# Kernel optimization log

Hardware: AMD Instinct MI355X
Metric: run time of the kernel (lower is better)

Reference implementation:

```python
import jax, jax.numpy as jnp
import numpy as np
from jax.ops import segment_sum, segment_max

B = 512          # parcels (batch of graphs)
P = 200          # poi nodes per parcel
N = B * P        # total poi nodes
E_POI = N * 16   # intra-parcel poi graph edges
HID = 256
IN_CH = 64
HEADS = 3
OUT = 12
T0 = 0.9
SLOPE = 0.2      # GATConv leaky_relu negative slope
NODE_GRAPH = jnp.arange(N, dtype=jnp.int32) // P  # poi node -> parcel id
ARANGE_N = jnp.arange(N, dtype=jnp.int32)


def setup_inputs() -> dict:
    key = jax.random.key(0)
    ks = jax.random.split(key, 24)
    g = lambda i, shape: jax.random.normal(ks[i], shape, jnp.float32) * 0.05
    # poi graph edges constrained within each parcel block
    src0 = jax.random.randint(ks[0], (E_POI,), 0, N, dtype=jnp.int32)
    off = jax.random.randint(ks[1], (E_POI,), 0, P, dtype=jnp.int32)
    return dict(
        g_poi_features=jax.random.normal(ks[2], (N, IN_CH), jnp.float32),
        img_feat=jax.random.normal(ks[3], (B, 2048), jnp.float32),
        edge_src=src0,
        edge_dst=(src0 // P) * P + off,
        W_gcn1=g(4, (IN_CH, HID)), b_gcn1=jnp.zeros((HID,), jnp.float32),
        W_gcn2=g(5, (HID, HID)), b_gcn2=jnp.zeros((HID,), jnp.float32),
        W_hrs=g(6, (2048, HID)), b_hrs=jnp.zeros((HID,), jnp.float32),
        W_proj_hrs=g(7, (HID, HID)), b_proj_hrs=jnp.zeros((HID,), jnp.float32),
        W_proj_poi=g(8, (HID, HID)), b_proj_poi=jnp.zeros((HID,), jnp.float32),
        W_gat_in=g(9, (HID, HEADS * HID)), al_in=g(10, (HEADS, HID)), ar_in=g(11, (HEADS, HID)),
        W_gat_with=g(12, (HID, HEADS * HID)), al_with=g(13, (HEADS, HID)), ar_with=g(14, (HEADS, HID)),
        W_hrsgnn=g(15, (HID, HID)),
        W_poignn=g(16, (HID, HID)),
        W_fc=g(17, (4 * HID, OUT)), b_fc=jnp.zeros((OUT,), jnp.float32),
    )


def _gcn(x, src, dst, W, b):
    # DGL GraphConv, norm='both', self-loops added
    s = jnp.concatenate([src, ARANGE_N])
    d = jnp.concatenate([dst, ARANGE_N])
    deg = segment_sum(jnp.ones_like(s, jnp.float32), d, num_segments=N)
    norm = jax.lax.rsqrt(jnp.maximum(deg, 1.0))
    h = (x @ W) * norm[:, None]
    m = segment_sum(h[s], d, num_segments=N)
    return m * norm[:, None] + b


def _gat(h_src, h_dst, src, dst, n_dst, W, al, ar):
    # DGL GATConv math: shared fc, additive attention, edge-softmax over dst
    fs = (h_src @ W).reshape(-1, HEADS, HID)
    fd = (h_dst @ W).reshape(-1, HEADS, HID)
    el = (fs * al).sum(-1)   # [n_src, H]
    er = (fd * ar).sum(-1)   # [n_dst, H]
    e = el[src] + er[dst]
    e = jnp.where(e > 0, e, SLOPE * e)
    m = segment_max(e, dst, num_segments=n_dst)
    w = jnp.exp(e - m[dst])
    z = segment_sum(w, dst, num_segments=n_dst)
    alpha = w / (z[dst] + 1e-9)
    out = segment_sum(fs[src] * alpha[:, :, None], dst, num_segments=n_dst)
    return out.mean(1)  # mean over heads (parcel_output.mean(1) in source)


def _mean_nodes(x):
    # dgl.mean_nodes over uniform-size batched graphs
    return segment_sum(x, NODE_GRAPH, num_segments=B) / P


def reference(g_poi_features, img_feat, edge_src, edge_dst,
              W_gcn1, b_gcn1, W_gcn2, b_gcn2, W_hrs, b_hrs,
              W_proj_hrs, b_proj_hrs, W_proj_poi, b_proj_poi,
              W_gat_in, al_in, ar_in, W_gat_with, al_with, ar_with,
              W_hrsgnn, W_poignn, W_fc, b_fc):
    # hrs_encoder: ResNet50 backbone modeled as precomputed 2048-d feats + replaced fc
    hrs = img_feat @ W_hrs + b_hrs                                  # [B, HID]
    # poi_encoder: 2-layer GCN over batched poi graph
    x = jax.nn.relu(_gcn(g_poi_features, edge_src, edge_dst, W_gcn1, b_gcn1))
    poi_nodes = _gcn(x, edge_src, edge_dst, W_gcn2, b_gcn2)         # [N, HID]
    poi_pooled = _mean_nodes(poi_nodes)                             # [B, HID]
    # mid-level fused similarity
    med = jnp.concatenate([hrs, poi_pooled], axis=1)
    med = med / jnp.linalg.norm(med, axis=1, keepdims=True)
    med_output = (med @ med.T + 1.0) / 2.0                          # [B, B]
    # UniSimGraph: GCN on thresholded parcel-similarity graph
    adj = jnp.where(med_output >= T0, 1.0, 0.0)
    adj = jnp.maximum(adj, jnp.eye(B, dtype=jnp.float32))
    dinv = jax.lax.rsqrt(adj.sum(1))
    nadj = adj * dinv[:, None] * dinv[None, :]
    hrs_agg = jax.nn.relu(nadj @ (hrs @ W_hrsgnn))                  # [B, HID]
    poi_agg = jax.nn.relu(nadj @ (poi_pooled @ W_poignn))           # [B, HID]
    # getHetGraph: bipartite poi<->parcel GAT, 3 heads, sum-aggregate, head-mean
    ph = hrs @ W_proj_hrs + b_proj_hrs                              # parcel feats
    pp = poi_nodes @ W_proj_poi + b_proj_poi                        # poi feats
    poi2img = _gat(pp, ph, ARANGE_N, NODE_GRAPH, B, W_gat_in, al_in, ar_in)      # [B, HID]
    img2poi = _gat(ph, pp, NODE_GRAPH, ARANGE_N, N, W_gat_with, al_with, ar_with)  # [N, HID]
    img2poi_pooled = _mean_nodes(img2poi)                           # [B, HID]
    # MutualAgg concat order: [img2poi, poi2poi(=poi_agg), poi2img, img2img(=hrs_agg)]
    agg = jnp.concatenate([img2poi_pooled, poi_agg, poi2img, hrs_agg], axis=1)
    output = agg @ W_fc + b_fc                                      # [B, OUT]
    return (output, med_output)
```

## Files before the change

### kernel.cpp

```cpp
#include <hip/hip_runtime.h>
#include <hip/hip_bf16.h>
#include <math.h>


#define N_NODES 102400
#define B_PAR   512
#define P_NODES 200
#define E_EDGES 1638400
#define HIDF    256

typedef __attribute__((ext_vector_type(8))) short bf16x8;
typedef __attribute__((ext_vector_type(4))) float f32x4;

__device__ __forceinline__ unsigned short f2bf(float x) {
    unsigned u = __builtin_bit_cast(unsigned, x);
    u += 0x7fffu + ((u >> 16) & 1u);
    return (unsigned short)(u >> 16);
}
__device__ __forceinline__ float bf2f(unsigned short h) {
    return __builtin_bit_cast(float, (unsigned)h << 16);
}
__device__ __forceinline__ int lds_off(int row, int kbyte) {
    return row * 128 + ((((kbyte >> 4) ^ (row & 7)) << 4) | (kbyte & 15));
}
template<bool BF16SRC>
__device__ __forceinline__ bf16x8 load_row8(const void* p, size_t elemoff) {
    if constexpr (BF16SRC) {
        return *(const bf16x8*)((const unsigned short*)p + elemoff);
    } else {
        const float* ap = (const float*)p + elemoff;
        float4 lo = *(const float4*)ap;
        float4 hi = *(const float4*)(ap + 4);
        union { bf16x8 v; unsigned short u[8]; } pk;
        pk.u[0] = f2bf(lo.x); pk.u[1] = f2bf(lo.y);
        pk.u[2] = f2bf(lo.z); pk.u[3] = f2bf(lo.w);
        pk.u[4] = f2bf(hi.x); pk.u[5] = f2bf(hi.y);
        pk.u[6] = f2bf(hi.z); pk.u[7] = f2bf(hi.w);
        return pk.v;
    }
}
__device__ __forceinline__ bf16x8 u8x8_to_bf16(uint2 w) {
    union { bf16x8 v; unsigned short u[8]; } r;
#pragma unroll
    for (int b = 0; b < 4; ++b) {
        r.u[b]     = (unsigned short)(__builtin_bit_cast(unsigned,
                        (float)((w.x >> (8 * b)) & 255u)) >> 16);
        r.u[4 + b] = (unsigned short)(__builtin_bit_cast(unsigned,
                        (float)((w.y >> (8 * b)) & 255u)) >> 16);
    }
    return r.v;
}

__global__ __launch_bounds__(512, 2) void gcnA_k(
    const unsigned char* __restrict__ Adj, const float* __restrict__ gp,
    const float* __restrict__ nrm, const unsigned short* __restrict__ W1t,
    const float* __restrict__ b1, unsigned short* __restrict__ X1nT)
{
    __shared__ unsigned short lds[256 * 72];
    unsigned short* XnT = lds;
    unsigned short* AX1 = lds;

    const int tid  = threadIdx.x;
    const int p    = blockIdx.x;
    const int lane = tid & 63;
    const int wave = tid >> 6;
    const int frow = lane & 15;
    const int fq   = lane >> 4;
    const int r4   = fq << 2;
    const f32x4 fz = {0.f, 0.f, 0.f, 0.f};

    uint2 adjr[2][7];
#pragma unroll
    for (int mi = 0; mi < 2; ++mi) {
        const unsigned char* ar = Adj + ((size_t)p << 16)
            + (size_t)(wave * 32 + mi * 16 + frow) * 256 + fq * 8;
#pragma unroll
        for (int ks = 0; ks < 7; ++ks)
            adjr[mi][ks] = *(const uint2*)(ar + ks * 32);
    }
    bf16x8 w1f[2][2];
#pragma unroll
    for (int mi = 0; mi < 2; ++mi)
#pragma unroll
        for (int ks = 0; ks < 2; ++ks)
            w1f[mi][ks] = *(const bf16x8*)(W1t
                + (size_t)(wave * 32 + mi * 16 + frow) * 64 + ks * 32 + fq * 8);

    for (int idx = tid; idx < 224 * 16; idx += 512) {
        int s = idx >> 4, kc = idx & 15;
        float4 v = {0.f, 0.f, 0.f, 0.f};
        float nr = 0.f;
        if (s < 200) {
            v = *(const float4*)(gp + ((size_t)(p * 200 + s)) * 64 + kc * 4);
            nr = nrm[p * 200 + s];
        }
        XnT[(kc * 4 + 0) * 232 + s] = f2bf(v.x * nr);
        XnT[(kc * 4 + 1) * 232 + s] = f2bf(v.y * nr);
        XnT[(kc * 4 + 2) * 232 + s] = f2bf(v.z * nr);
        XnT[(kc * 4 + 3) * 232 + s] = f2bf(v.w * nr);
    }
    __syncthreads();

    f32x4 acc2[2][4];
#pragma unroll
    for (int i = 0; i < 2; ++i)
#pragma unroll
        for (int j = 0; j < 4; ++j) acc2[i][j] = fz;
#pragma unroll
    for (int ks = 0; ks < 7; ++ks) {
        bf16x8 a0 = u8x8_to_bf16(adjr[0][ks]);
        bf16x8 a1 = u8x8_to_bf16(adjr[1][ks]);
#pragma unroll
        for (int ni = 0; ni < 4; ++ni) {
            bf16x8 bfr = *(const bf16x8*)(XnT
                + (size_t)(ni * 16 + frow) * 232 + ks * 32 + fq * 8);
            acc2[0][ni] = __builtin_amdgcn_mfma_f32_16x16x32_bf16(a0, bfr, acc2[0][ni], 0, 0, 0);
            acc2[1][ni] = __builtin_amdgcn_mfma_f32_16x16x32_bf16(a1, bfr, acc2[1][ni], 0, 0, 0);
        }
    }
    __syncthreads();
#pragma unroll
    for (int mi = 0; mi < 2; ++mi)
#pragma unroll
        for (int ni = 0; ni < 4; ++ni)
#pragma unroll
            for (int j = 0; j < 4; ++j)
                AX1[(size_t)(wave * 32 + mi * 16 + r4 + j) * 72 + ni * 16 + frow]
                    = f2bf(acc2[mi][ni][j]);
    __syncthreads();

    f32x4 acc3[2][16];
#pragma unroll
    for (int i = 0; i < 2; ++i)
#pragma unroll
        for (int j = 0; j < 16; ++j) acc3[i][j] = fz;
#pragma unroll
    for (int ks = 0; ks < 2; ++ks)
#pragma unroll
        for (int ni = 0; ni < 16; ++ni) {
            bf16x8 bfr = *(const bf16x8*)(AX1
                + (size_t)(ni * 16 + frow) * 72 + ks * 32 + fq * 8);
            acc3[0][ni] = __builtin_amdgcn_mfma_f32_16x16x32_bf16(w1f[0][ks], bfr, acc3[0][ni], 0, 0, 0);
            acc3[1][ni] = __builtin_amdgcn_mfma_f32_16x16x32_bf16(w1f[1][ks], bfr, acc3[1][ni], 0, 0, 0);
        }

    float nrd[16];
#pragma unroll
    for (int ni = 0; ni < 16; ++ni) {
        int d = ni * 16 + frow;
        nrd[ni] = (d < 200) ? nrm[p * 200 + d] : 0.f;
    }
#pragma unroll
    for (int mi = 0; mi < 2; ++mi)
#pragma unroll
        for (int j = 0; j < 4; ++j) {
            int f = wave * 32 + mi * 16 + r4 + j;
            float bv = b1[f];
#pragma unroll
            for (int ni = 0; ni < 16; ++ni) {
                int d = ni * 16 + frow;
                if (d < 224) {
                    float v = fmaxf(acc3[mi][ni][j] * nrd[ni] + bv, 0.f) * nrd[ni];
                    X1nT[((size_t)p * 256 + f) * 224 + d] = f2bf(v);
                }
            }
        }
}

__global__ __launch_bounds__(512, 2) void gcnB_k(
    const unsigned char* __restrict__ Adj, const unsigned short* __restrict__ X1nT,
    const unsigned short* __restrict__ W2t, const float* __restrict__ nrm,
    const float* __restrict__ b2, unsigned short* __restrict__ PN,
    float* __restrict__ pool, unsigned short* __restrict__ poolb)
{
    __shared__ unsigned short Bb[32 * 232];
    __shared__ unsigned short AXb[256 * 40];
    __shared__ unsigned short W2b[256 * 40];
    __shared__ float poolsh[256];

    const int tid  = threadIdx.x;
    const int p    = blockIdx.x;
    const int lane = tid & 63;
    const int wave = tid >> 6;
    const int frow = lane & 15;
    const int fq   = lane >> 4;
    const int r4   = fq << 2;
    const f32x4 fz = {0.f, 0.f, 0.f, 0.f};

    if (tid < 256) poolsh[tid] = 0.f;

    bf16x8 adjb[2][7];
#pragma unroll
    for (int mi = 0; mi < 2; ++mi) {
        const unsigned char* ar = Adj + ((size_t)p << 16)
            + (size_t)(wave * 32 + mi * 16 + frow) * 256 + fq * 8;
#pragma unroll
        for (int ks = 0; ks < 7; ++ks)
            adjb[mi][ks] = u8x8_to_bf16(*(const uint2*)(ar + ks * 32));
    }

    f32x4 acc5[2][16];
#pragma unroll
    for (int i = 0; i < 2; ++i)
#pragma unroll
        for (int j = 0; j < 16; ++j) acc5[i][j] = fz;

#pragma unroll
    for (int i = 0; i < 2; ++i) {
        int idx = tid + i * 512;
        if (idx < 896) {
            int r = idx / 28, ch = idx - r * 28;
            *(uint4*)(Bb + r * 232 + ch * 8) =
                *(const uint4*)(X1nT + ((size_t)p * 256 + r) * 224 + ch * 8);
        }
        int r2 = idx >> 2, ch2 = idx & 3;
        *(uint4*)(W2b + r2 * 40 + ch2 * 8) =
            *(const uint4*)(W2t + (size_t)r2 * 256 + ch2 * 8);
    }
    __syncthreads();

    for (int c = 0; c < 8; ++c) {
        uint4 stb[2];
#pragma unroll
        for (int i = 0; i < 2; ++i) {
            int idx = tid + i * 512;
            if (c < 7 && idx < 896) {
                int r = idx / 28, ch = idx - r * 28;
                stb[i] = *(const uint4*)(X1nT
                    + ((size_t)p * 256 + (c + 1) * 32 + r) * 224 + ch * 8);
            }
        }
        f32x4 acc4[2][2];
#pragma unroll
        for (int i = 0; i < 2; ++i)
#pragma unroll
            for (int j = 0; j < 2; ++j) acc4[i][j] = fz;
#pragma unroll
        for (int ks = 0; ks < 7; ++ks)
#pragma unroll
            for (int ni = 0; ni < 2; ++ni) {
                bf16x8 bfr = *(const bf16x8*)(Bb
                    + (size_t)(ni * 16 + frow) * 232 + ks * 32 + fq * 8);
                acc4[0][ni] = __builtin_amdgcn_mfma_f32_16x16x32_bf16(adjb[0][ks], bfr, acc4[0][ni], 0, 0, 0);
                acc4[1][ni] = __builtin_amdgcn_mfma_f32_16x16x32_bf16(adjb[1][ks], bfr, acc4[1][ni], 0, 0, 0);
            }
        __syncthreads();
#pragma unroll
        for (int mi = 0; mi < 2; ++mi)
#pragma unroll
            for (int ni = 0; ni < 2; ++ni)
#pragma unroll
                for (int j = 0; j < 4; ++j)
                    AXb[(size_t)(wave * 32 + mi * 16 + r4 + j) * 40 + ni * 16 + frow]
                        = f2bf(acc4[mi][ni][j]);
#pragma unroll
        for (int i = 0; i < 2; ++i) {
            int idx = tid + i * 512;
            if (c < 7 && idx < 896) {
                int r = idx / 28, ch = idx - r * 28;
                *(uint4*)(Bb + r * 232 + ch * 8) = stb[i];
            }
        }
        __syncthreads();
        uint4 stw[2];
#pragma unroll
        for (int i = 0; i < 2; ++i) {
            int idx = tid + i * 512;
            int r = idx >> 2, ch = idx & 3;
            if (c < 7)
                stw[i] = *(const uint4*)(W2t
                    + (size_t)r * 256 + (c + 1) * 32 + ch * 8);
        }
        bf16x8 af[2];
        af[0] = *(const bf16x8*)(AXb + (size_t)(wave * 32 + frow) * 40 + fq * 8);
        af[1] = *(const bf16x8*)(AXb + (size_t)(wave * 32 + 16 + frow) * 40 + fq * 8);
#pragma unroll
        for (int ni = 0; ni < 16; ++ni) {
            bf16x8 bfr = *(const bf16x8*)(W2b + (size_t)(ni * 16 + frow) * 40 + fq * 8);
            acc5[0][ni] = __builtin_amdgcn_mfma_f32_16x16x32_bf16(af[0], bfr, acc5[0][ni], 0, 0, 0);
            acc5[1][ni] = __builtin_amdgcn_mfma_f32_16x16x32_bf16(af[1], bfr, acc5[1][ni], 0, 0, 0);
        }
        __syncthreads();
#pragma unroll
        for (int i = 0; i < 2; ++i) {
            int idx = tid + i * 512;
            int r = idx >> 2, ch = idx & 3;
            if (c < 7) *(uint4*)(W2b + r * 40 + ch * 8) = stw[i];
        }
    }

    float b2v[16], psum[16];
#pragma unroll
    for (int ni = 0; ni < 16; ++ni) {
        b2v[ni] = b2[ni * 16 + frow];
        psum[ni] = 0.f;
    }
#pragma unroll
    for (int mi = 0; mi < 2; ++mi)
#pragma unroll
        for (int j = 0; j < 4; ++j) {
            int d = wave * 32 + mi * 16 + r4 + j;
            if (d < 200) {
                int g = p * 200 + d;
                float nr = nrm[g];
#pragma unroll
                for (int ni = 0; ni < 16; ++ni) {
                    float v = acc5[mi][ni][j] * nr + b2v[ni];
                    PN[(size_t)g * 256 + ni * 16 + frow] = f2bf(v);
                    psum[ni] += v;
                }
            }
        }
#pragma unroll
    for (int ni = 0; ni < 16; ++ni) {
        float s = psum[ni];
        s += __shfl_xor(s, 16);
        s += __shfl_xor(s, 32);
        if (fq == 0) atomicAdd(&poolsh[ni * 16 + frow], s);
    }
    __syncthreads();
    if (tid < 256) {
        float pv = poolsh[tid] * (1.f / 200.f);
        pool[(size_t)p * 256 + tid] = pv;
        poolb[(size_t)p * 256 + tid] = f2bf(pv);
    }
}

template<bool ABF16, bool BBF16, int OMODE, bool BIASF, bool RELUF,
         bool MEDOUT, int KCHUNK>
__global__ __launch_bounds__(256) void mm64_k(
    const void* __restrict__ Ain, const void* __restrict__ Bin,
    void* __restrict__ Cout, int M, int Nc, int K,
    const float* __restrict__ bias, float alpha)
{
    __shared__ bf16x8 smem_v[1024];
    unsigned char* Asm = (unsigned char*)smem_v;
    unsigned char* Bsm = Asm + 8192;

    const int tid  = threadIdx.x;
    const int m0   = blockIdx.y * 64;
    const int n0   = blockIdx.x * 64;
    const int sr   = tid >> 3, sc = tid & 7;
    const int lane = tid & 63;
    const int wm   = (tid >> 7) & 1, wn = (tid >> 6) & 1;
    const int frow = lane & 15;
    const int fko  = (lane >> 4) << 4;

    int kbeg = 0, kend = K;
    float* Cf = (float*)Cout;
    if (KCHUNK > 0) {
        kbeg = blockIdx.z * KCHUNK; kend = kbeg + KCHUNK;
        Cf += (size_t)blockIdx.z * M * Nc;
    }

    f32x4 acc[2][2];
    const f32x4 fz = {0.f, 0.f, 0.f, 0.f};
#pragma unroll
    for (int i = 0; i < 2; ++i)
#pragma unroll
        for (int j = 0; j < 2; ++j) acc[i][j] = fz;

    bf16x8 areg[2], breg[2];
    auto load_tiles = [&](int k0) {
#pragma unroll
        for (int i = 0; i < 2; ++i) {
            int row = sr + 32 * i;
            areg[i] = load_row8<ABF16>(Ain, (size_t)(m0 + row) * K + k0 + sc * 8);
            breg[i] = load_row8<BBF16>(Bin, (size_t)(n0 + row) * K + k0 + sc * 8);
        }
    };

    load_tiles(kbeg);
    for (int k0 = kbeg; k0 < kend; k0 += 64) {
        __syncthreads();
#pragma unroll
        for (int i = 0; i < 2; ++i) {
            *(bf16x8*)(Asm + lds_off(sr + 32 * i, sc * 16)) = areg[i];
            *(bf16x8*)(Bsm + lds_off(sr + 32 * i, sc * 16)) = breg[i];
        }
        __syncthreads();
        if (k0 + 64 < kend) load_tiles(k0 + 64);
#pragma unroll
        for (int ks = 0; ks < 2; ++ks) {
            const int kb = ks * 64 + fko;
            bf16x8 af[2], bfr[2];
#pragma unroll
            for (int t = 0; t < 2; ++t)
                af[t] = *(const bf16x8*)(Asm + lds_off(wm * 32 + t * 16 + frow, kb));
#pragma unroll
            for (int t = 0; t < 2; ++t)
                bfr[t] = *(const bf16x8*)(Bsm + lds_off(wn * 32 + t * 16 + frow, kb));
#pragma unroll
            for (int mi = 0; mi < 2; ++mi)
#pragma unroll
                for (int ni = 0; ni < 2; ++ni)
                    acc[mi][ni] = __builtin_amdgcn_mfma_f32_16x16x32_bf16(
                        af[mi], bfr[ni], acc[mi][ni], 0, 0, 0);
        }
    }

    const int r4 = (lane >> 4) << 2;
#pragma unroll
    for (int mi = 0; mi < 2; ++mi) {
#pragma unroll
        for (int ni = 0; ni < 2; ++ni) {
            int col = n0 + wn * 32 + ni * 16 + frow;
#pragma unroll
            for (int j = 0; j < 4; ++j) {
                int row = m0 + wm * 32 + mi * 16 + r4 + j;
                float v = acc[mi][ni][j] * alpha;
                if (BIASF)  v += bias[col];
                if (RELUF)  v = fmaxf(v, 0.f);
                if (MEDOUT) v += 0.5f;
                if (OMODE == 0) {
                    Cf[(size_t)row * Nc + col] = v;
                } else {
                    ((unsigned short*)Cout)[(size_t)row * Nc + col] = f2bf(v);
                }
            }
        }
    }
}

__global__ __launch_bounds__(256) void edge_diag_k(
    const int* __restrict__ esrc, const int* __restrict__ edst,
    unsigned char* __restrict__ A)
{
    int id = blockIdx.x * 256 + threadIdx.x;
    size_t bo;
    if (id < E_EDGES) {
        int s = esrc[id], d = edst[id];
        int p = d / 200;
        int dl = d - p * 200, sl = s - p * 200;
        bo = (((size_t)(p * 256 + dl)) << 8) + (unsigned)sl;
    } else {
        int i2 = id - E_EDGES;
        int p = i2 / 200, d = i2 - p * 200;
        bo = (((size_t)(p * 256 + d)) << 8) + (unsigned)d;
    }
    atomicAdd((unsigned int*)(A + (bo & ~(size_t)3)), 1u << ((bo & 3) * 8));
}

__global__ __launch_bounds__(256) void norm2_k(const unsigned char* __restrict__ A,
                                               float* __restrict__ nrm)
{
    int g = blockIdx.x * 256 + threadIdx.x;
    int p = g / 200, d = g - p * 200;
    const uint4* row = (const uint4*)(A + (((size_t)(p * 256 + d)) << 8));
    unsigned s = 0;
#pragma unroll
    for (int i = 0; i < 16; ++i) {
        uint4 w = row[i];
        unsigned a = w.x, b = w.y, c = w.z, e = w.w;
        s += (a & 255) + ((a >> 8) & 255) + ((a >> 16) & 255) + (a >> 24);
        s += (b & 255) + ((b >> 8) & 255) + ((b >> 16) & 255) + (b >> 24);
        s += (c & 255) + ((c >> 8) & 255) + ((c >> 16) & 255) + (c >> 24);
        s += (e & 255) + ((e >> 8) & 255) + ((e >> 16) & 255) + (e >> 24);
    }
    nrm[g] = rsqrtf((float)s);
}

__global__ __launch_bounds__(256) void prep_k(
    const float* __restrict__ W1, const float* __restrict__ W2,
    const float* __restrict__ Whg,
    const float* __restrict__ Wpg, const float* __restrict__ Whrs,
    const float* __restrict__ Wgin, const float* __restrict__ Wgw,
    const float* __restrict__ Wph, const float* __restrict__ img,
    unsigned short* __restrict__ W1t, unsigned short* __restrict__ W2t,
    unsigned short* __restrict__ Whgt,
    unsigned short* __restrict__ Wpgt, unsigned short* __restrict__ Whrst,
    unsigned short* __restrict__ Wgint, unsigned short* __restrict__ Wmt,
    unsigned short* __restrict__ Wphb, unsigned short* __restrict__ imgb)
{
    int b = blockIdx.x, tid = threadIdx.x;
    if (b < 64) {
        int id = b * 256 + tid; int n = id >> 6, k = id & 63;
        W1t[id] = f2bf(W1[(size_t)k * 256 + n]);
// ... 51 lines not shown
        bgg[j] = s * (1.f / 3.f);
    }
}

__global__ __launch_bounds__(256) void hrs_reduce_k(
    const float* __restrict__ part, const float* __restrict__ bhrs,
    float* __restrict__ hrs, unsigned short* __restrict__ hrsb)
{
    int id = blockIdx.x * 256 + threadIdx.x;
    float s = bhrs[id & 255];
#pragma unroll
    for (int z = 0; z < 8; ++z) s += part[(size_t)z * 131072 + id];
    hrs[id] = s;
    hrsb[id] = f2bf(s);
}

__global__ __launch_bounds__(256) void med_build_k(
    const float* __restrict__ hrs, const float* __restrict__ pool,
    unsigned short* __restrict__ medb)
{
    __shared__ float red[256];
    int b = blockIdx.x, f = threadIdx.x;
    float v0 = hrs[(size_t)b * 256 + f];
    float v1 = pool[(size_t)b * 256 + f];
    red[f] = v0 * v0 + v1 * v1;
    __syncthreads();
    for (int s = 128; s > 0; s >>= 1) {
        if (f < s) red[f] += red[f + s];
        __syncthreads();
    }
    float inv = rsqrtf(red[0]);
    medb[(size_t)b * 512 + f]       = f2bf(v0 * inv);
    medb[(size_t)b * 512 + 256 + f] = f2bf(v1 * inv);
}

__global__ __launch_bounds__(256) void dinv_k(const float* __restrict__ mo,
                                              float* __restrict__ dinv)
{
    __shared__ int red[256];
    int i = blockIdx.x, t = threadIdx.x;
    int c = 0;
    for (int j = t; j < 512; j += 256) c += (mo[(size_t)i * 512 + j] >= 0.9f) ? 1 : 0;
    red[t] = c; __syncthreads();
    for (int s = 128; s > 0; s >>= 1) {
        if (t < s) red[t] += red[t + s];
        __syncthreads();
    }
    if (t == 0) dinv[i] = rsqrtf((float)red[0]);
}

__global__ __launch_bounds__(256) void nadj_k(const float* __restrict__ mo,
                                              const float* __restrict__ dinv,
                                              unsigned short* __restrict__ nadjb)
{
    int i = blockIdx.x, t = threadIdx.x;
    float di = dinv[i];
    for (int j = t; j < 512; j += 256) {
        float a = (mo[(size_t)i * 512 + j] >= 0.9f || j == i) ? 1.f : 0.f;
        nadjb[(size_t)i * 512 + j] = f2bf(a * di * dinv[j]);
    }
}

__global__ __launch_bounds__(256) void uv1_k(
    const float* __restrict__ Wgin, const float* __restrict__ al,
    const float* __restrict__ ar,
    float* __restrict__ u2, float* __restrict__ v2)
{
    const int wave = threadIdx.x >> 6, lane = threadIdx.x & 63;
    const int task = blockIdx.x * 4 + wave;
    const int k = task / 3, h = task - k * 3;
    float4 w = *(const float4*)(Wgin + (size_t)k * 768 + h * 256 + lane * 4);
    float4 a = *(const float4*)(al + h * 256 + lane * 4);
    float4 r = *(const float4*)(ar + h * 256 + lane * 4);
    float su = w.x * a.x + w.y * a.y + w.z * a.z + w.w * a.w;
    float sv = w.x * r.x + w.y * r.y + w.z * r.z + w.w * r.w;
#pragma unroll
    for (int o = 32; o > 0; o >>= 1) {
        su += __shfl_xor(su, o);
        sv += __shfl_xor(sv, o);
    }
    if (lane == 0) { u2[task] = su; v2[task] = sv; }
}

__global__ __launch_bounds__(256) void uv2_k(
    const float* __restrict__ Wph, const float* __restrict__ Wpp,
    const float* __restrict__ bph, const float* __restrict__ bpp,
    const unsigned short* __restrict__ Wmt,
    const float* __restrict__ u2, const float* __restrict__ v2,
    float* __restrict__ vv2, float* __restrict__ wu,
    float* __restrict__ bc, float* __restrict__ erb, float* __restrict__ eb0)
{
    __shared__ float ush[768], vsh[768];
    const int tid = threadIdx.x;
    for (int i = tid; i < 768; i += 256) { ush[i] = u2[i]; vsh[i] = v2[i]; }
    __syncthreads();
    const int wave = tid >> 6, lane = tid & 63;
    const int task = blockIdx.x * 4 + wave;
    float s = 0.f;
    if (task < 1536) {
        int t2 = task < 768 ? task : task - 768;
        int k = t2 / 3, h = t2 - k * 3;
        const float* W = task < 768 ? Wph : Wpp;
        const float* vec = task < 768 ? vsh : ush;
        float4 w = *(const float4*)(W + (size_t)k * 256 + lane * 4);
        s = w.x * vec[(lane * 4 + 0) * 3 + h] + w.y * vec[(lane * 4 + 1) * 3 + h]
          + w.z * vec[(lane * 4 + 2) * 3 + h] + w.w * vec[(lane * 4 + 3) * 3 + h];
#pragma unroll
        for (int o = 32; o > 0; o >>= 1) s += __shfl_xor(s, o);
        if (lane == 0) { if (task < 768) vv2[t2] = s; else wu[t2] = s; }
    } else if (task < 1792) {
        int k = task - 1536;
        float4 b4 = *(const float4*)(bph + lane * 4);
        const unsigned short* wm = Wmt + (size_t)k * 256 + lane * 4;
        s = b4.x * bf2f(wm[0]) + b4.y * bf2f(wm[1])
          + b4.z * bf2f(wm[2]) + b4.w * bf2f(wm[3]);
#pragma unroll
        for (int o = 32; o > 0; o >>= 1) s += __shfl_xor(s, o);
        if (lane == 0) bc[k] = s;
    } else if (task < 1798) {
        int t2 = task - 1792;
        int h = t2 % 3;
        bool second = t2 >= 3;
        const float* bias = second ? bpp : bph;
        const float* vec  = second ? ush : vsh;
        float4 b4 = *(const float4*)(bias + lane * 4);
        s = b4.x * vec[(lane * 4 + 0) * 3 + h] + b4.y * vec[(lane * 4 + 1) * 3 + h]
          + b4.z * vec[(lane * 4 + 2) * 3 + h] + b4.w * vec[(lane * 4 + 3) * 3 + h];
#pragma unroll
        for (int o = 32; o > 0; o >>= 1) s += __shfl_xor(s, o);
        if (lane == 0) { if (second) eb0[h] = s; else erb[h] = s; }
    }
}

__global__ __launch_bounds__(256) void er2_k(
    const float* __restrict__ hrs, const float* __restrict__ vv2,
    const float* __restrict__ erb, const float* __restrict__ eb0,
    float* __restrict__ er)
{
    __shared__ float vsh[768];
    const int tid = threadIdx.x;
    for (int i = tid; i < 768; i += 256) vsh[i] = vv2[i];
    __syncthreads();
    const int wave = tid >> 6, lane = tid & 63;
    const int task = blockIdx.x * 4 + wave;
    const int b = task / 3, h = task - b * 3;
    float4 hv = *(const float4*)(hrs + (size_t)b * 256 + lane * 4);
    float s = hv.x * vsh[(lane * 4 + 0) * 3 + h] + hv.y * vsh[(lane * 4 + 1) * 3 + h]
            + hv.z * vsh[(lane * 4 + 2) * 3 + h] + hv.w * vsh[(lane * 4 + 3) * 3 + h];
#pragma unroll
    for (int o = 32; o > 0; o >>= 1) s += __shfl_xor(s, o);
    if (lane == 0) er[task] = erb[h] + eb0[h] + s;
}

__global__ __launch_bounds__(256) void gat_poi2img_k(
    const unsigned short* __restrict__ PN, const float* __restrict__ wu,
    const float* __restrict__ er, float* __restrict__ q)
{
    __shared__ float esh[600];
    __shared__ float ash[600];
    __shared__ float ush[768];
    __shared__ float mz[8];
    const int p = blockIdx.x, tid = threadIdx.x;
    const size_t base = (size_t)p * P_NODES;

    for (int i = tid; i < 768; i += 256) ush[i] = wu[i];
    __syncthreads();

    for (int it = tid; it < 600; it += 256) {
        int n = it / 3, h = it % 3;
        const unsigned short* row = PN + (base + n) * HIDF;
        float s = 0.f;
        for (int k = 0; k < 256; k += 8) {
            union { uint4 qv; unsigned short us[8]; } w;
            w.qv = *(const uint4*)(row + k);
#pragma unroll
            for (int j = 0; j < 8; ++j) s += bf2f(w.us[j]) * ush[(k + j) * 3 + h];
        }
        s += er[p * 3 + h];
        esh[it] = s > 0.f ? s : 0.2f * s;
    }
    __syncthreads();

    int wave = tid >> 6, lane = tid & 63;
    if (wave < 3) {
        float mx = -1e30f;
        for (int n = lane; n < P_NODES; n += 64) mx = fmaxf(mx, esh[n * 3 + wave]);
        for (int o = 32; o > 0; o >>= 1) mx = fmaxf(mx, __shfl_xor(mx, o));
        float sm = 0.f;
        for (int n = lane; n < P_NODES; n += 64) sm += expf(esh[n * 3 + wave] - mx);
        for (int o = 32; o > 0; o >>= 1) sm += __shfl_xor(sm, o);
        if (lane == 0) { mz[wave] = mx; mz[4 + wave] = sm; }
    }
    __syncthreads();

    for (int it = tid; it < 600; it += 256) {
        int h = it % 3;
        ash[it] = expf(esh[it] - mz[h]) / (mz[4 + h] + 1e-9f);
    }
    __syncthreads();

    float a0 = 0.f, a1 = 0.f, a2 = 0.f;
    for (int n = 0; n < P_NODES; ++n) {
        float vv = bf2f(PN[(base + n) * HIDF + tid]);
        a0 += ash[n * 3 + 0] * vv;
        a1 += ash[n * 3 + 1] * vv;
        a2 += ash[n * 3 + 2] * vv;
    }
    q[((size_t)p * 3 + 0) * 256 + tid] = a0;
    q[((size_t)p * 3 + 1) * 256 + tid] = a1;
    q[((size_t)p * 3 + 2) * 256 + tid] = a2;
}

__global__ __launch_bounds__(256) void final_k(
    const float* __restrict__ i2p, const float* __restrict__ hpagg,
    const float* __restrict__ p2i,
    const float* __restrict__ Wfc, const float* __restrict__ bfc,
    float* __restrict__ out)
{
    int id = blockIdx.x * 256 + threadIdx.x;
    if (id >= B_PAR * 12) return;
    int b = id / 12, o = id % 12;
    float acc = bfc[o];
    const float* s0 = i2p + (size_t)b * 256;
    const float* s1 = hpagg + (size_t)b * 512 + 256;
    const float* s2 = p2i + (size_t)b * 256;
    const float* s3 = hpagg + (size_t)b * 512;
    for (int k = 0; k < 256; ++k) {
        acc += s0[k] * Wfc[(size_t)(0 * 256 + k) * 12 + o];
        acc += s1[k] * Wfc[(size_t)(1 * 256 + k) * 12 + o];
        acc += s2[k] * Wfc[(size_t)(2 * 256 + k) * 12 + o];
        acc += s3[k] * Wfc[(size_t)(3 * 256 + k) * 12 + o];
    }
    out[id] = acc;
}

extern "C" void kernel_launch(void* const* d_in, const int* in_sizes, int n_in,
                              void* d_out, int out_size, void* d_ws, size_t ws_size,
                              hipStream_t stream)
{
    const float* g_poi = (const float*)d_in[0];
    const float* img   = (const float*)d_in[1];
    const int*   esrc  = (const int*)d_in[2];
    const int*   edst  = (const int*)d_in[3];
    const float* W1    = (const float*)d_in[4];
    const float* b1    = (const float*)d_in[5];
    const float* W2    = (const float*)d_in[6];
    const float* b2    = (const float*)d_in[7];
    const float* Whrs  = (const float*)d_in[8];
    const float* bhrs  = (const float*)d_in[9];
    const float* Wph   = (const float*)d_in[10];
    const float* bph   = (const float*)d_in[11];
    const float* Wpp   = (const float*)d_in[12];
    const float* bpp   = (const float*)d_in[13];
    const float* Wgin  = (const float*)d_in[14];
    const float* alin  = (const float*)d_in[15];
    const float* arin  = (const float*)d_in[16];
    const float* Wgw   = (const float*)d_in[17];
    const float* Whg   = (const float*)d_in[20];
    const float* Wpg   = (const float*)d_in[21];
    const float* Wfc   = (const float*)d_in[22];
    const float* bfc   = (const float*)d_in[23];

    float* out     = (float*)d_out;
    float* med_out = out + B_PAR * 12;

    char* ws = (char*)d_ws;
    size_t off = 0;
    auto take = [&](size_t bytes) { void* pv = ws + off; off += (bytes + 255) & ~(size_t)255; return pv; };

    unsigned char*  adj8 = (unsigned char*)take((size_t)B_PAR * 256 * 256);
    unsigned short* X1nT = (unsigned short*)take((size_t)B_PAR * 256 * 224 * 2);
    unsigned short* XPN  = (unsigned short*)take((size_t)N_NODES * 256 * 2);
    float*          part = (float*)take((size_t)8 * 512 * 256 * 4);

    unsigned short* W1t   = (unsigned short*)take(256 * 64 * 2);
    unsigned short* W2t   = (unsigned short*)take(256 * 256 * 2);
    unsigned short* Whgt  = (unsigned short*)take(256 * 256 * 2);
    unsigned short* Wpgt  = (unsigned short*)take(256 * 256 * 2);
    unsigned short* Whrst = (unsigned short*)take((size_t)256 * 2048 * 2);
    unsigned short* Wgint = (unsigned short*)take((size_t)256 * 768 * 2);
    unsigned short* Wmt   = (unsigned short*)take(256 * 256 * 2);
    unsigned short* Wphb  = (unsigned short*)take(256 * 256 * 2);
    unsigned short* WcT   = (unsigned short*)take(256 * 256 * 2);
    unsigned short* WpG   = (unsigned short*)take((size_t)256 * 768 * 2);
    unsigned short* imgb  = (unsigned short*)take((size_t)512 * 2048 * 2);
    unsigned short* hrsb  = (unsigned short*)take((size_t)B_PAR * 256 * 2);
    unsigned short* poolb = (unsigned short*)take((size_t)B_PAR * 256 * 2);
    unsigned short* medb  = (unsigned short*)take((size_t)B_PAR * 512 * 2);
    unsigned short* nadjb = (unsigned short*)take((size_t)B_PAR * 512 * 2);
    unsigned short* Tcatt = (unsigned short*)take((size_t)512 * 512 * 2);
    float* nrm   = (float*)take((size_t)N_NODES * 4);
    float* hrs   = (float*)take((size_t)B_PAR * 256 * 4);
    float* pool  = (float*)take((size_t)B_PAR * 256 * 4);
    float* dinv  = (float*)take((size_t)B_PAR * 4);
    float* hpagg = (float*)take((size_t)B_PAR * 512 * 4);
    float* u2    = (float*)take(768 * 4);
    float* v2    = (float*)take(768 * 4);
    float* wu    = (float*)take(768 * 4);
    float* vv2   = (float*)take(768 * 4);
    float* erb   = (float*)take(16);
    float* eb0   = (float*)take(16);
    float* bc    = (float*)take(256 * 4);
    float* bgg   = (float*)take(256 * 4);
    float* er    = (float*)take((size_t)B_PAR * 3 * 4);
    float* q     = (float*)take((size_t)B_PAR * 768 * 4);
    float* p2i   = (float*)take((size_t)B_PAR * 256 * 4);
    float* i2p   = (float*)take((size_t)B_PAR * 256 * 4);
    (void)ws_size; (void)in_sizes; (void)n_in; (void)out_size;

    hipMemsetAsync(adj8, 0, (size_t)B_PAR * 256 * 256, stream);
    prep_k<<<8256, 256, 0, stream>>>(W1, W2, Whg, Wpg, Whrs, Wgin, Wgw,
        Wph, img, W1t, W2t, Whgt, Wpgt, Whrst, Wgint, Wmt, Wphb, imgb);
    edge_diag_k<<<(E_EDGES + N_NODES) / 256, 256, 0, stream>>>(esrc, edst, adj8);
    norm2_k<<<N_NODES / 256, 256, 0, stream>>>(adj8, nrm);
    wpg_k<<<769, 256, 0, stream>>>(Wpp, Wgin, bpp, WpG, bgg);

    mm64_k<true, true, 0, false, false, false, 256>
        <<<dim3(4, 8, 8), 256, 0, stream>>>(imgb, Whrst, part, 512, 256, 2048,
            nullptr, 1.f);
    hrs_reduce_k<<<512, 256, 0, stream>>>(part, bhrs, hrs, hrsb);

    uv1_k<<<192, 256, 0, stream>>>(Wgin, alin, arin, u2, v2);
    uv2_k<<<450, 256, 0, stream>>>(Wph, Wpp, bph, bpp, Wmt, u2, v2,
                                   vv2, wu, bc, erb, eb0);
    er2_k<<<384, 256, 0, stream>>>(hrs, vv2, erb, eb0, er);
    mm64_k<true, true, 1, false, false, false, 0>
        <<<dim3(4, 4), 256, 0, stream>>>(Wmt, Wphb, WcT, 256, 256, 256,
            nullptr, 1.f);

    gcnA_k<<<B_PAR, 512, 0, stream>>>(adj8, g_poi, nrm, W1t, b1, X1nT);
    gcnB_k<<<B_PAR, 512, 0, stream>>>(adj8, X1nT, W2t, nrm, b2, XPN,
                                      pool, poolb);

    med_build_k<<<B_PAR, 256, 0, stream>>>(hrs, pool, medb);
    mm64_k<true, true, 0, false, false, true, 0>
        <<<dim3(8, 8), 256, 0, stream>>>(medb, medb, med_out, 512, 512, 512,
            nullptr, 0.5f);

    dinv_k<<<B_PAR, 256, 0, stream>>>(med_out, dinv);
    nadj_k<<<B_PAR, 256, 0, stream>>>(med_out, dinv, nadjb);
    mm64_k<true, true, 1, false, false, false, 0>
        <<<dim3(8, 4), 256, 0, stream>>>(Whgt, hrsb, Tcatt, 256, 512, 256,
            nullptr, 1.f);
    mm64_k<true, true, 1, false, false, false, 0>
        <<<dim3(8, 4), 256, 0, stream>>>(Wpgt, poolb, Tcatt + (size_t)256 * 512,
            256, 512, 256, nullptr, 1.f);
    mm64_k<true, true, 0, false, true, false, 0>
        <<<dim3(8, 8), 256, 0, stream>>>(nadjb, Tcatt, hpagg, 512, 512, 512,
            nullptr, 1.f);

    gat_poi2img_k<<<B_PAR, 256, 0, stream>>>(XPN, wu, er, q);
    mm64_k<false, true, 0, true, false, false, 0>
        <<<dim3(4, 8), 256, 0, stream>>>(q, WpG, p2i, 512, 256, 768,
            bgg, 1.f / 3.f);

    mm64_k<true, true, 0, true, false, false, 0>
        <<<dim3(4, 8), 256, 0, stream>>>(hrsb, WcT, i2p, 512, 256, 256,
            bc, 1.f);

    final_k<<<24, 256, 0, stream>>>(i2p, hpagg, p2i, Wfc, bfc, out);
}
```

Before: 391.6 us.

## Fuse GAT poi-to-parcel attention into second GCN kernel and swizzle LDS layouts

```diff
diff --git a/kernel.cpp b/kernel.cpp
--- a/kernel.cpp
+++ b/kernel.cpp
@@ -22,6 +22,9 @@
 }
 __device__ __forceinline__ int lds_off(int row, int kbyte) {
     return row * 128 + ((((kbyte >> 4) ^ (row & 7)) << 4) | (kbyte & 15));
+}
+__device__ __forceinline__ int w2off(int row, int kbyte) {
+    return row * 64 + (((((kbyte >> 4) & 3) ^ (row & 3)) << 4) | (kbyte & 15));
 }
 template<bool BF16SRC>
 __device__ __forceinline__ bf16x8 load_row8(const void* p, size_t elemoff) {
@@ -50,15 +53,20 @@
     }
     return r.v;
 }
+__device__ __forceinline__ unsigned long long pack4bf(f32x4 v) {
+    union { unsigned long long u; unsigned short h[4]; } pk;
+    pk.h[0] = f2bf(v[0]); pk.h[1] = f2bf(v[1]);
+    pk.h[2] = f2bf(v[2]); pk.h[3] = f2bf(v[3]);
+    return pk.u;
+}
 
 __global__ __launch_bounds__(512, 2) void gcnA_k(
     const unsigned char* __restrict__ Adj, const float* __restrict__ gp,
     const float* __restrict__ nrm, const unsigned short* __restrict__ W1t,
     const float* __restrict__ b1, unsigned short* __restrict__ X1nT)
 {
-    __shared__ unsigned short lds[256 * 72];
-    unsigned short* XnT = lds;
-    unsigned short* AX1 = lds;
+    __shared__ unsigned char XnU[32768];
+    __shared__ unsigned char AXU[32768];
 
     const int tid  = threadIdx.x;
     const int p    = blockIdx.x;
@@ -86,60 +94,52 @@
             w1f[mi][ks] = *(const bf16x8*)(W1t
                 + (size_t)(wave * 32 + mi * 16 + frow) * 64 + ks * 32 + fq * 8);
 
-    for (int idx = tid; idx < 224 * 16; idx += 512) {
-        int s = idx >> 4, kc = idx & 15;
-        float4 v = {0.f, 0.f, 0.f, 0.f};
-        float nr = 0.f;
-        if (s < 200) {
-            v = *(const float4*)(gp + ((size_t)(p * 200 + s)) * 64 + kc * 4);
-            nr = nrm[p * 200 + s];
-        }
-        XnT[(kc * 4 + 0) * 232 + s] = f2bf(v.x * nr);
-        XnT[(kc * 4 + 1) * 232 + s] = f2bf(v.y * nr);
-        XnT[(kc * 4 + 2) * 232 + s] = f2bf(v.z * nr);
-        XnT[(kc * 4 + 3) * 232 + s] = f2bf(v.w * nr);
+    for (int gi = wave; gi < 28; gi += 8) {
+        int s0 = gi * 8;
+        union { bf16x8 v; unsigned short h[8]; } pk;
+#pragma unroll
+        for (int t = 0; t < 8; ++t) {
+            int s = s0 + t;
+            float val = 0.f;
+            if (s < 200)
+                val = gp[((size_t)(p * 200 + s)) * 64 + lane] * nrm[p * 200 + s];
+            pk.h[t] = f2bf(val);
+        }
+        *(bf16x8*)(XnU + lds_off((s0 >> 6) * 64 + lane, (s0 & 63) * 2)) = pk.v;
     }
     __syncthreads();
 
-    f32x4 acc2[2][4];
+#pragma unroll
+    for (int mi_d = 0; mi_d < 2; ++mi_d) {
+        bf16x8 adjf[7];
+#pragma unroll
+        for (int ks = 0; ks < 7; ++ks) adjf[ks] = u8x8_to_bf16(adjr[mi_d][ks]);
+#pragma unroll
+        for (int kt = 0; kt < 4; ++kt) {
+            f32x4 a2 = fz;
+#pragma unroll
+            for (int ks = 0; ks < 7; ++ks) {
+                bf16x8 af = *(const bf16x8*)(XnU + lds_off(
+                    (ks >> 1) * 64 + kt * 16 + frow, ((ks & 1) * 32 + fq * 8) * 2));
+                a2 = __builtin_amdgcn_mfma_f32_16x16x32_bf16(af, adjf[ks], a2, 0, 0, 0);
+            }
+            *(unsigned long long*)(AXU + lds_off(
+                wave * 32 + mi_d * 16 + frow, kt * 32 + fq * 8)) = pack4bf(a2);
+        }
+    }
+    __syncthreads();
+
+    f32x4 acc3[2][16];
 #pragma unroll
     for (int i = 0; i < 2; ++i)
 #pragma unroll
-        for (int j = 0; j < 4; ++j) acc2[i][j] = fz;
-#pragma unroll
-    for (int ks = 0; ks < 7; ++ks) {
-        bf16x8 a0 = u8x8_to_bf16(adjr[0][ks]);
-        bf16x8 a1 = u8x8_to_bf16(adjr[1][ks]);
-#pragma unroll
-        for (int ni = 0; ni < 4; ++ni) {
-            bf16x8 bfr = *(const bf16x8*)(XnT
-                + (size_t)(ni * 16 + frow) * 232 + ks * 32 + fq * 8);
-            acc2[0][ni] = __builtin_amdgcn_mfma_f32_16x16x32_bf16(a0, bfr, acc2[0][ni], 0, 0, 0);
-            acc2[1][ni] = __builtin_amdgcn_mfma_f32_16x16x32_bf16(a1, bfr, acc2[1][ni], 0, 0, 0);
-        }
-    }
-    __syncthreads();
-#pragma unroll
-    for (int mi = 0; mi < 2; ++mi)
-#pragma unroll
-        for (int ni = 0; ni < 4; ++ni)
-#pragma unroll
-            for (int j = 0; j < 4; ++j)
-                AX1[(size_t)(wave * 32 + mi * 16 + r4 + j) * 72 + ni * 16 + frow]
-                    = f2bf(acc2[mi][ni][j]);
-    __syncthreads();
-
-    f32x4 acc3[2][16];
-#pragma unroll
-    for (int i = 0; i < 2; ++i)
-#pragma unroll
         for (int j = 0; j < 16; ++j) acc3[i][j] = fz;
 #pragma unroll
     for (int ks = 0; ks < 2; ++ks)
 #pragma unroll
         for (int ni = 0; ni < 16; ++ni) {
-            bf16x8 bfr = *(const bf16x8*)(AX1
-                + (size_t)(ni * 16 + frow) * 72 + ks * 32 + fq * 8);
+            bf16x8 bfr = *(const bf16x8*)(AXU + lds_off(
+                ni * 16 + frow, ks * 64 + fq * 16));
             acc3[0][ni] = __builtin_amdgcn_mfma_f32_16x16x32_bf16(w1f[0][ks], bfr, acc3[0][ni], 0, 0, 0);
             acc3[1][ni] = __builtin_amdgcn_mfma_f32_16x16x32_bf16(w1f[1][ks], bfr, acc3[1][ni], 0, 0, 0);
         }
@@ -167,16 +167,18 @@
         }
 }
 
-__global__ __launch_bounds__(512, 2) void gcnB_k(
+__global__ __launch_bounds__(512, 2) void gcnBG_k(
     const unsigned char* __restrict__ Adj, const unsigned short* __restrict__ X1nT,
     const unsigned short* __restrict__ W2t, const float* __restrict__ nrm,
-    const float* __restrict__ b2, unsigned short* __restrict__ PN,
+    const float* __restrict__ b2, const float* __restrict__ er,
+    const float* __restrict__ wu, float* __restrict__ qout,
     float* __restrict__ pool, unsigned short* __restrict__ poolb)
 {
-    __shared__ unsigned short Bb[32 * 232];
-    __shared__ unsigned short AXb[256 * 40];
-    __shared__ unsigned short W2b[256 * 40];
-    __shared__ float poolsh[256];
+    __shared__ unsigned char BbU[16384];
+    __shared__ unsigned char AXbU[32768];
+    __shared__ unsigned char W2bU[16384];
+    __shared__ float wush[768];
+    __shared__ float mz[8];
 
     const int tid  = threadIdx.x;
     const int p    = blockIdx.x;
@@ -187,8 +189,6 @@
     const int r4   = fq << 2;
     const f32x4 fz = {0.f, 0.f, 0.f, 0.f};
 
-    if (tid < 256) poolsh[tid] = 0.f;
-
     bf16x8 adjb[2][7];
 #pragma unroll
     for (int mi = 0; mi < 2; ++mi) {
@@ -199,130 +199,214 @@
             adjb[mi][ks] = u8x8_to_bf16(*(const uint2*)(ar + ks * 32));
     }
 
+    for (int i = tid; i < 768; i += 512) wush[i] = wu[i];
+
     f32x4 acc5[2][16];
 #pragma unroll
     for (int i = 0; i < 2; ++i)
 #pragma unroll
         for (int j = 0; j < 16; ++j) acc5[i][j] = fz;
 
-#pragma unroll
-    for (int i = 0; i < 2; ++i) {
-        int idx = tid + i * 512;
-        if (idx < 896) {
-            int r = idx / 28, ch = idx - r * 28;
-            *(uint4*)(Bb + r * 232 + ch * 8) =
-                *(const uint4*)(X1nT + ((size_t)p * 256 + r) * 224 + ch * 8);
-        }
-        int r2 = idx >> 2, ch2 = idx & 3;
-        *(uint4*)(W2b + r2 * 40 + ch2 * 8) =
-            *(const uint4*)(W2t + (size_t)r2 * 256 + ch2 * 8);
-    }
-    __syncthreads();
-
-    for (int c = 0; c < 8; ++c) {
-        uint4 stb[2];
+    auto bbDst = [&](int idx) {
+        int fl = idx / 28, soct = idx - fl * 28;
+        int s0 = soct * 8;
+        return lds_off((s0 >> 6) * 32 + fl, (s0 & 63) * 2);
+    };
+    auto bbSrc = [&](int c, int idx) {
+        int fl = idx / 28, soct = idx - fl * 28;
+        return (const uint4*)(X1nT + ((size_t)p * 256 + c * 32 + fl) * 224 + soct * 8);
+    };
+
+    {
+        *(uint4*)(BbU + bbDst(tid)) = *bbSrc(0, tid);
+        if (tid < 384) *(uint4*)(BbU + bbDst(tid + 512)) = *bbSrc(0, tid + 512);
 #pragma unroll
         for (int i = 0; i < 2; ++i) {
             int idx = tid + i * 512;
-            if (c < 7 && idx < 896) {
-                int r = idx / 28, ch = idx - r * 28;
-                stb[i] = *(const uint4*)(X1nT
-                    + ((size_t)p * 256 + (c + 1) * 32 + r) * 224 + ch * 8);
+            int r = idx >> 2, oct = idx & 3;
+            *(uint4*)(W2bU + w2off(r, oct * 16)) =
+                *(const uint4*)(W2t + (size_t)r * 256 + oct * 8);
+        }
+    }
+    __syncthreads();
+
+    for (int c = 0; c < 8; ++c) {
+        uint4 stb0, stb1;
+        if (c < 7) {
+            stb0 = *bbSrc(c + 1, tid);
+            if (tid < 384) stb1 = *bbSrc(c + 1, tid + 512);
+        }
+        f32x4 acc4[2][2];
+#pragma unroll
+        for (int i = 0; i < 2; ++i)
+#pragma unroll
+            for (int j = 0; j < 2; ++j) acc4[i][j] = fz;
+#pragma unroll
+        for (int ks = 0; ks < 7; ++ks) {
+#pragma unroll
+            for (int mi_f = 0; mi_f < 2; ++mi_f) {
+                bf16x8 af = *(const bf16x8*)(BbU + lds_off(
+                    (ks >> 1) * 32 + mi_f * 16 + frow, ((ks & 1) * 32 + fq * 8) * 2));
+                acc4[0][mi_f] = __builtin_amdgcn_mfma_f32_16x16x32_bf16(af, adjb[0][ks], acc4[0][mi_f], 0, 0, 0);
+                acc4[1][mi_f] = __builtin_amdgcn_mfma_f32_16x16x32_bf16(af, adjb[1][ks], acc4[1][mi_f], 0, 0, 0);
             }
         }
-        f32x4 acc4[2][2];
-#pragma unroll
-        for (int i = 0; i < 2; ++i)
-#pragma unroll
-            for (int j = 0; j < 2; ++j) acc4[i][j] = fz;
-#pragma unroll
-        for (int ks = 0; ks < 7; ++ks)
-#pragma unroll
-            for (int ni = 0; ni < 2; ++ni) {
-                bf16x8 bfr = *(const bf16x8*)(Bb
-                    + (size_t)(ni * 16 + frow) * 232 + ks * 32 + fq * 8);
-                acc4[0][ni] = __builtin_amdgcn_mfma_f32_16x16x32_bf16(adjb[0][ks], bfr, acc4[0][ni], 0, 0, 0);
-                acc4[1][ni] = __builtin_amdgcn_mfma_f32_16x16x32_bf16(adjb[1][ks], bfr, acc4[1][ni], 0, 0, 0);
-            }
         __syncthreads();
 #pragma unroll
-        for (int mi = 0; mi < 2; ++mi)
-#pragma unroll
-            for (int ni = 0; ni < 2; ++ni)
-#pragma unroll
-                for (int j = 0; j < 4; ++j)
-                    AXb[(size_t)(wave * 32 + mi * 16 + r4 + j) * 40 + ni * 16 + frow]
-                        = f2bf(acc4[mi][ni][j]);
-#pragma unroll
-        for (int i = 0; i < 2; ++i) {
-            int idx = tid + i * 512;
-            if (c < 7 && idx < 896) {
-                int r = idx / 28, ch = idx - r * 28;
-                *(uint4*)(Bb + r * 232 + ch * 8) = stb[i];
-            }
+        for (int mi_d = 0; mi_d < 2; ++mi_d)
+#pragma unroll
+            for (int mi_f = 0; mi_f < 2; ++mi_f)
+                *(unsigned long long*)(AXbU + lds_off(
+                    wave * 32 + mi_d * 16 + frow, mi_f * 32 + fq * 8))
+                    = pack4bf(acc4[mi_d][mi_f]);
+        if (c < 7) {
+            *(uint4*)(BbU + bbDst(tid)) = stb0;
+            if (tid < 384) *(uint4*)(BbU + bbDst(tid + 512)) = stb1;
         }
         __syncthreads();
         uint4 stw[2];
-#pragma unroll
-        for (int i = 0; i < 2; ++i) {
-            int idx = tid + i * 512;
-            int r = idx >> 2, ch = idx & 3;
-            if (c < 7)
-                stw[i] = *(const uint4*)(W2t
-                    + (size_t)r * 256 + (c + 1) * 32 + ch * 8);
-        }
-        bf16x8 af[2];
-        af[0] = *(const bf16x8*)(AXb + (size_t)(wave * 32 + frow) * 40 + fq * 8);
-        af[1] = *(const bf16x8*)(AXb + (size_t)(wave * 32 + 16 + frow) * 40 + fq * 8);
+        if (c < 7) {
+#pragma unroll
+            for (int i = 0; i < 2; ++i) {
+                int idx = tid + i * 512;
+                int r = idx >> 2, oct = idx & 3;
+                stw[i] = *(const uint4*)(W2t + (size_t)r * 256 + (c + 1) * 32 + oct * 8);
+            }
+        }
+        bf16x8 a5[2];
+        a5[0] = *(const bf16x8*)(AXbU + lds_off(wave * 32 + frow, fq * 16));
+        a5[1] = *(const bf16x8*)(AXbU + lds_off(wave * 32 + 16 + frow, fq * 16));
 #pragma unroll
         for (int ni = 0; ni < 16; ++ni) {
-            bf16x8 bfr = *(const bf16x8*)(W2b + (size_t)(ni * 16 + frow) * 40 + fq * 8);
-            acc5[0][ni] = __builtin_amdgcn_mfma_f32_16x16x32_bf16(af[0], bfr, acc5[0][ni], 0, 0, 0);
-            acc5[1][ni] = __builtin_amdgcn_mfma_f32_16x16x32_bf16(af[1], bfr, acc5[1][ni], 0, 0, 0);
+            bf16x8 bfr = *(const bf16x8*)(W2bU + w2off(ni * 16 + frow, fq * 16));
+            acc5[0][ni] = __builtin_amdgcn_mfma_f32_16x16x32_bf16(a5[0], bfr, acc5[0][ni], 0, 0, 0);
+            acc5[1][ni] = __builtin_amdgcn_mfma_f32_16x16x32_bf16(a5[1], bfr, acc5[1][ni], 0, 0, 0);
         }
         __syncthreads();
-#pragma unroll
-        for (int i = 0; i < 2; ++i) {
-            int idx = tid + i * 512;
-            int r = idx >> 2, ch = idx & 3;
-            if (c < 7) *(uint4*)(W2b + r * 40 + ch * 8) = stw[i];
-        }
-    }
-
-    float b2v[16], psum[16];
-#pragma unroll
-    for (int ni = 0; ni < 16; ++ni) {
-        b2v[ni] = b2[ni * 16 + frow];
-        psum[ni] = 0.f;
-    }
+        if (c < 7) {
+#pragma unroll
+            for (int i = 0; i < 2; ++i) {
+                int idx = tid + i * 512;
+                int r = idx >> 2, oct = idx & 3;
+                *(uint4*)(W2bU + w2off(r, oct * 16)) = stw[i];
+            }
+        }
+    }
+
+    float* esh = (float*)BbU;
+    float* qsh = (float*)AXbU;
+
+    float b2v[16], nrv[2][4];
+#pragma unroll
+    for (int ni = 0; ni < 16; ++ni) b2v[ni] = b2[ni * 16 + frow];
 #pragma unroll
     for (int mi = 0; mi < 2; ++mi)
 #pragma unroll
         for (int j = 0; j < 4; ++j) {
             int d = wave * 32 + mi * 16 + r4 + j;
-            if (d < 200) {
-                int g = p * 200 + d;
-                float nr = nrm[g];
-#pragma unroll
-                for (int ni = 0; ni < 16; ++ni) {
-                    float v = acc5[mi][ni][j] * nr + b2v[ni];
-                    PN[(size_t)g * 256 + ni * 16 + frow] = f2bf(v);
-                    psum[ni] += v;
-                }
+            nrv[mi][j] = (d < 200) ? nrm[p * 200 + d] : 0.f;
+        }
+    float er3[3];
+#pragma unroll
+    for (int h = 0; h < 3; ++h) er3[h] = er[p * 3 + h];
+
+#pragma unroll
+    for (int mi = 0; mi < 2; ++mi)
+#pragma unroll
+        for (int j = 0; j < 4; ++j) {
+            float e0 = 0.f, e1 = 0.f, e2 = 0.f;
+            float nr = nrv[mi][j];
+#pragma unroll
+            for (int ni = 0; ni < 16; ++ni) {
+                float vv = acc5[mi][ni][j] * nr + b2v[ni];
+                int wb = (ni * 16 + frow) * 3;
+                e0 += vv * wush[wb];
+                e1 += vv * wush[wb + 1];
+                e2 += vv * wush[wb + 2];
             }
-        }
-#pragma unroll
-    for (int ni = 0; ni < 16; ++ni) {
-        float s = psum[ni];
-        s += __shfl_xor(s, 16);
-        s += __shfl_xor(s, 32);
-        if (fq == 0) atomicAdd(&poolsh[ni * 16 + frow], s);
-    }
+#pragma unroll
+            for (int o = 1; o < 16; o <<= 1) {
+                e0 += __shfl_xor(e0, o);
+                e1 += __shfl_xor(e1, o);
+                e2 += __shfl_xor(e2, o);
+            }
+            int d = wave * 32 + mi * 16 + r4 + j;
+            if (frow == 0 && d < 200) {
+                float t0 = e0 + er3[0]; t0 = t0 > 0.f ? t0 : 0.2f * t0;
+                float t1 = e1 + er3[1]; t1 = t1 > 0.f ? t1 : 0.2f * t1;
+                float t2 = e2 + er3[2]; t2 = t2 > 0.f ? t2 : 0.2f * t2;
+                esh[d * 3 + 0] = t0;
+                esh[d * 3 + 1] = t1;
+                esh[d * 3 + 2] = t2;
+            }
+        }
     __syncthreads();
-    if (tid < 256) {
-        float pv = poolsh[tid] * (1.f / 200.f);
-        pool[(size_t)p * 256 + tid] = pv;
-        poolb[(size_t)p * 256 + tid] = f2bf(pv);
+
+    if (wave < 3) {
+        float mx = -1e30f;
+        for (int n = lane; n < 200; n += 64) mx = fmaxf(mx, esh[n * 3 + wave]);
+#pragma unroll
+        for (int o = 32; o > 0; o >>= 1) mx = fmaxf(mx, __shfl_xor(mx, o));
+        float sm = 0.f;
+        for (int n = lane; n < 200; n += 64) sm += expf(esh[n * 3 + wave] - mx);
+#pragma unroll
+        for (int o = 32; o > 0; o >>= 1) sm += __shfl_xor(sm, o);
+        if (lane == 0) { mz[wave] = mx; mz[4 + wave] = sm; }
+    }
+    __syncthreads();
+
+    float alph[2][4][3];
+#pragma unroll
+    for (int mi = 0; mi < 2; ++mi)
+#pragma unroll
+        for (int j = 0; j < 4; ++j) {
+            int d = wave * 32 + mi * 16 + r4 + j;
+#pragma unroll
+            for (int h = 0; h < 3; ++h)
+                alph[mi][j][h] = (d < 200)
+                    ? expf(esh[d * 3 + h] - mz[h]) / (mz[4 + h] + 1e-9f) : 0.f;
+        }
+
+#pragma unroll
+    for (int cfn = 0; cfn < 4; ++cfn) {
+        float qacc[16];
+#pragma unroll
+        for (int ni = 0; ni < 16; ++ni) qacc[ni] = 0.f;
+        float csum = 0.f;
+#pragma unroll
+        for (int mi = 0; mi < 2; ++mi)
+#pragma unroll
+            for (int j = 0; j < 4; ++j) {
+                int d = wave * 32 + mi * 16 + r4 + j;
+                float coef = 0.f;
+                if (d < 200) coef = (cfn < 3) ? alph[mi][j][cfn] : 0.005f;
+                float cn = coef * nrv[mi][j];
+                csum += coef;
+#pragma unroll
+                for (int ni = 0; ni < 16; ++ni)
+                    qacc[ni] += cn * acc5[mi][ni][j];
+            }
+#pragma unroll
+        for (int ni = 0; ni < 16; ++ni) {
+            float v = qacc[ni] + csum * b2v[ni];
+            v += __shfl_xor(v, 16);
+            v += __shfl_xor(v, 32);
+            if (fq == 0) qsh[wave * 1024 + cfn * 256 + ni * 16 + frow] = v;
+        }
+    }
+    __syncthreads();
+
+    for (int i = tid; i < 1024; i += 512) {
+        int cfn = i >> 8, f = i & 255;
+        float s = 0.f;
+#pragma unroll
+        for (int w = 0; w < 8; ++w) s += qsh[w * 1024 + cfn * 256 + f];
+        if (cfn < 3) {
+            qout[(size_t)p * 768 + cfn * 256 + f] = s;
+        } else {
+            pool[(size_t)p * 256 + f] = s;
+            poolb[(size_t)p * 256 + f] = f2bf(s);
+        }
     }
 }
 
@@ -680,65 +764,6 @@
     if (lane == 0) er[task] = erb[h] + eb0[h] + s;
 }
 
-__global__ __launch_bounds__(256) void gat_poi2img_k(
-    const unsigned short* __restrict__ PN, const float* __restrict__ wu,
-    const float* __restrict__ er, float* __restrict__ q)
-{
-    __shared__ float esh[600];
-    __shared__ float ash[600];
-    __shared__ float ush[768];
-    __shared__ float mz[8];
-    const int p = blockIdx.x, tid = threadIdx.x;
-    const size_t base = (size_t)p * P_NODES;
-
-    for (int i = tid; i < 768; i += 256) ush[i] = wu[i];
-    __syncthreads();
-
-    for (int it = tid; it < 600; it += 256) {
-        int n = it / 3, h = it % 3;
-        const unsigned short* row = PN + (base + n) * HIDF;
-        float s = 0.f;
-        for (int k = 0; k < 256; k += 8) {
-            union { uint4 qv; unsigned short us[8]; } w;
-            w.qv = *(const uint4*)(row + k);
-#pragma unroll
-            for (int j = 0; j < 8; ++j) s += bf2f(w.us[j]) * ush[(k + j) * 3 + h];
-        }
-        s += er[p * 3 + h];
-        esh[it] = s > 0.f ? s : 0.2f * s;
-    }
-    __syncthreads();
-
-    int wave = tid >> 6, lane = tid & 63;
-    if (wave < 3) {
-        float mx = -1e30f;
-        for (int n = lane; n < P_NODES; n += 64) mx = fmaxf(mx, esh[n * 3 + wave]);
-        for (int o = 32; o > 0; o >>= 1) mx = fmaxf(mx, __shfl_xor(mx, o));
-        float sm = 0.f;
-        for (int n = lane; n < P_NODES; n += 64) sm += expf(esh[n * 3 + wave] - mx);
-        for (int o = 32; o > 0; o >>= 1) sm += __shfl_xor(sm, o);
-        if (lane == 0) { mz[wave] = mx; mz[4 + wave] = sm; }
-    }
-    __syncthreads();
-
-    for (int it = tid; it < 600; it += 256) {
-        int h = it % 3;
-        ash[it] = expf(esh[it] - mz[h]) / (mz[4 + h] + 1e-9f);
-    }
-    __syncthreads();
-
-    float a0 = 0.f, a1 = 0.f, a2 = 0.f;
-    for (int n = 0; n < P_NODES; ++n) {
-        float vv = bf2f(PN[(base + n) * HIDF + tid]);
-        a0 += ash[n * 3 + 0] * vv;
-        a1 += ash[n * 3 + 1] * vv;
-        a2 += ash[n * 3 + 2] * vv;
-    }
-    q[((size_t)p * 3 + 0) * 256 + tid] = a0;
-    q[((size_t)p * 3 + 1) * 256 + tid] = a1;
-    q[((size_t)p * 3 + 2) * 256 + tid] = a2;
-}
-
 __global__ __launch_bounds__(256) void final_k(
     const float* __restrict__ i2p, const float* __restrict__ hpagg,
     const float* __restrict__ p2i,
@@ -798,7 +823,6 @@
 
     unsigned char*  adj8 = (unsigned char*)take((size_t)B_PAR * 256 * 256);
     unsigned short* X1nT = (unsigned short*)take((size_t)B_PAR * 256 * 224 * 2);
-    unsigned short* XPN  = (unsigned short*)take((size_t)N_NODES * 256 * 2);
     float*          part = (float*)take((size_t)8 * 512 * 256 * 4);
 
     unsigned short* W1t   = (unsigned short*)take(256 * 64 * 2);
@@ -857,8 +881,8 @@
             nullptr, 1.f);
 
     gcnA_k<<<B_PAR, 512, 0, stream>>>(adj8, g_poi, nrm, W1t, b1, X1nT);
-    gcnB_k<<<B_PAR, 512, 0, stream>>>(adj8, X1nT, W2t, nrm, b2, XPN,
-                                      pool, poolb);
+    gcnBG_k<<<B_PAR, 512, 0, stream>>>(adj8, X1nT, W2t, nrm, b2, er, wu,
+                                       q, pool, poolb);
 
     med_build_k<<<B_PAR, 256, 0, stream>>>(hrs, pool, medb);
     mm64_k<true, true, 0, false, false, true, 0>
@@ -877,7 +901,6 @@
         <<<dim3(8, 8), 256, 0, stream>>>(nadjb, Tcatt, hpagg, 512, 512, 512,
             nullptr, 1.f);
 
-    gat_poi2img_k<<<B_PAR, 256, 0, stream>>>(XPN, wu, er, q);
     mm64_k<false, true, 0, true, false, false, 0>
         <<<dim3(4, 8), 256, 0, stream>>>(q, WpG, p2i, 512, 256, 768,
             bgg, 1.f / 3.f);
```

Measured after the change: 367.0 us. 6.3% less time.
